# Performance work log

Hardware: AMD Instinct MI355X
Metric: run time of the kernel (lower is better)

## Reference

```python
import jax, jax.numpy as jnp
import numpy as np

R, DIL = 3, 2  # radius, dilation for neighbor correlation


def conv2d(x, w, b):
    # standard 3x3 stride-1 SAME conv, NCHW / OIHW
    y = jax.lax.conv_general_dilated(x, w, (1, 1), 'SAME',
                                     dimension_numbers=('NCHW', 'OIHW', 'NCHW'))
    return y + b[None, :, None, None]


def bilinear_gather(x, py, px):
    # x: (n,c,h,w); py/px: (n,K,h,w) float sampling coords; zero outside bounds
    n, c, h, w = x.shape
    y0 = jnp.floor(py); x0 = jnp.floor(px)
    wy = py - y0; wx = px - x0
    xf = x.reshape(n, c, h * w)

    def gather(yi, xi):
        valid = ((yi >= 0) & (yi < h) & (xi >= 0) & (xi < w)).astype(x.dtype)
        yc = jnp.clip(yi, 0, h - 1).astype(jnp.int32)
        xc = jnp.clip(xi, 0, w - 1).astype(jnp.int32)
        idx = (yc * w + xc).reshape(n, -1)  # (n, K*h*w)
        v = jax.vmap(lambda f, i: f[:, i])(xf, idx)  # (n, c, K*h*w)
        return v.reshape(n, c, *yi.shape[1:]) * valid[:, None]

    v00 = gather(y0, x0); v01 = gather(y0, x0 + 1)
    v10 = gather(y0 + 1, x0); v11 = gather(y0 + 1, x0 + 1)
    wy_ = wy[:, None]; wx_ = wx[:, None]
    return (v00 * (1 - wy_) * (1 - wx_) + v01 * (1 - wy_) * wx_
            + v10 * wy_ * (1 - wx_) + v11 * wy_ * wx_)


def dcn(x, w, b, ow, ob):
    # DCNv2-style modulated deformable 3x3 conv, stride 1, pad 1, 1 deformable group.
    # Offset/mask predicted by an internal conv: channels = [dy(9), dx(9), mask(9)].
    n, c, h, w_ = x.shape
    K = 9
    om = conv2d(x, ow, ob)  # (n, 27, h, w)
    dy, dx = om[:, :K], om[:, K:2 * K]
    mask = jax.nn.sigmoid(om[:, 2 * K:])
    ky, kx = jnp.meshgrid(jnp.arange(-1, 2), jnp.arange(-1, 2), indexing='ij')
    ky = ky.reshape(K).astype(x.dtype); kx = kx.reshape(K).astype(x.dtype)
    yy = jnp.arange(h, dtype=x.dtype)[None, None, :, None]
    xx = jnp.arange(w_, dtype=x.dtype)[None, None, None, :]
    py = yy + ky[None, :, None, None] + dy  # (n,K,h,w)
    px = xx + kx[None, :, None, None] + dx
    samp = bilinear_gather(x, py, px) * mask[:, None]  # (n,c,K,h,w)
    return jnp.einsum('nckhw,ock->nohw', samp, w.reshape(w.shape[0], c, K)) + b[None, :, None, None]


def ncf(f1, f2, radius, dilation):
    # neighbor_correlation_filter: unfold-based sliding-window dot-product attention
    n, c, h, w = f2.shape
    k = 2 * radius + 1
    pad = (k - 1) * dilation // 2
    f2p = jnp.pad(f2, ((0, 0), (0, 0), (pad, pad), (pad, pad)))
    # (n,c,K,h,w), tap order (ky outer, kx inner) matching F.unfold row-major layout
    patches = jnp.stack([f2p[:, :, i * dilation:i * dilation + h, j * dilation:j * dilation + w]
                         for i in range(k) for j in range(k)], axis=2)
    corr = jnp.einsum('nchw,nckhw->nkhw', f1, patches) / jnp.sqrt(jnp.asarray(c, f1.dtype))
    attn = jax.nn.softmax(corr, axis=1)
    sample = jnp.einsum('nkhw,nckhw->nchw', attn, patches)
    return sample, corr


def stargru(x, t, zw, zb, zow, zob, hw, hb, how, hob):
    tx = jnp.concatenate([x, t], axis=1)
    z = jax.nn.sigmoid(dcn(tx, zw, zb, zow, zob))
    r, _ = ncf(t, x, R, DIL)
    xt = jnp.tanh(dcn(jnp.concatenate([r, t], axis=1), hw, hb, how, hob))
    return (1.0 - z) * t + z * xt


def setup_inputs():
    key = jax.random.key(0)
    N, CIN, CH, H, W = 2, 256, 64, 96, 96
    ks = iter(jax.random.split(key, 32))

    def rn(shape, s=0.05):
        return jax.random.normal(next(ks), shape, jnp.float32) * s

    inp = {
        'x': jax.random.normal(next(ks), (N, CIN, H, W), jnp.float32),
        'template': jax.random.normal(next(ks), (N, CH, H, W), jnp.float32),
        'w_in': rn((CH, CIN, 3, 3)), 'b_in': jnp.zeros((CH,), jnp.float32),
        'w_out': rn((CIN, CH, 3, 3)), 'b_out': jnp.zeros((CIN,), jnp.float32),
    }
    for pre in ('enh_z', 'enh_h', 'upd_z', 'upd_h'):
        inp[pre + '_w'] = rn((CH, 2 * CH, 3, 3))
        inp[pre + '_b'] = jnp.zeros((CH,), jnp.float32)
        inp[pre + '_ow'] = rn((27, 2 * CH, 3, 3), 0.01)  # offset/mask conv (small init)
        inp[pre + '_ob'] = jnp.zeros((27,), jnp.float32)
    return inp


def reference(x, template, w_in, b_in, w_out, b_out,
              enh_z_w, enh_z_b, enh_z_ow, enh_z_ob,
              enh_h_w, enh_h_b, enh_h_ow, enh_h_ob,
              upd_z_w, upd_z_b, upd_z_ow, upd_z_ob,
              upd_h_w, upd_h_b, upd_h_ow, upd_h_ob):
    # CrossUpdate forward, post-first-frame branch (self.template is not None)
    xh = conv2d(x, w_in, b_in)
    x_enh = stargru(template, xh,
                    enh_z_w, enh_z_b, enh_z_ow, enh_z_ob,
                    enh_h_w, enh_h_b, enh_h_ow, enh_h_ob)
    new_template = stargru(xh, template,
                           upd_z_w, upd_z_b, upd_z_ow, upd_z_ob,
                           upd_h_w, upd_h_b, upd_h_ow, upd_h_ob)
    out = conv2d(x_enh, w_out, b_out)
    return (out, new_template)
```

## Files before the change

kernel.cpp:

```cpp
#include <hip/hip_runtime.h>
#include <hip/hip_bf16.h>

typedef __hip_bfloat16 bf16;
typedef unsigned short u16;
typedef unsigned int u32;
typedef __attribute__((ext_vector_type(8))) short short8;
typedef __attribute__((ext_vector_type(4))) short bh4;
typedef __attribute__((ext_vector_type(4))) float floatx4;

constexpr int N_ = 2, H_ = 96, W_ = 96, HW_ = H_ * W_;
constexpr int CIN_ = 256, CH_ = 64, C2_ = 128;

__device__ __forceinline__ float sigm(float v) { return 1.0f / (1.0f + __expf(-v)); }
__device__ __forceinline__ short f2b(float v) { bf16 h = __float2bfloat16(v); return *reinterpret_cast<short*>(&h); }
__device__ __forceinline__ float b2f(short s) {
    union { u32 i; float f; } v; v.i = ((u32)(u16)s) << 16; return v.f;
}

constexpr int A_IN_OFF = 0,                         A_IN_SZ  = 64 * 2304;
constexpr int A_OUT_OFF = A_IN_OFF + A_IN_SZ,       A_OUT_SZ = 256 * 576;
constexpr int A_OFF_OFF = A_OUT_OFF + A_OUT_SZ,     A_OFF_SZ = 64 * 1152;
constexpr int A_DCN_OFF = A_OFF_OFF + 4 * A_OFF_SZ, A_DCN_SZ = 64 * 1152;
constexpr int A_TOT = A_DCN_OFF + 4 * A_DCN_SZ;

__global__ __launch_bounds__(256) void cvt_weights(
        const float* __restrict__ w_in, const float* __restrict__ w_out,
        const float* __restrict__ ow0, const float* __restrict__ ow1,
        const float* __restrict__ ow2, const float* __restrict__ ow3,
        const float* __restrict__ w0, const float* __restrict__ w1,
        const float* __restrict__ w2, const float* __restrict__ w3,
        u16* __restrict__ dst) {
    int id = blockIdx.x * 256 + threadIdx.x;
    if (id >= A_TOT) return;
    float v;
    if (id < A_OUT_OFF) {
        int l = id; int m = l / 2304, k = l % 2304; int tap = k >> 8, ic = k & 255;
        v = w_in[m * 2304 + ic * 9 + tap];
    } else if (id < A_OFF_OFF) {
        int l = id - A_OUT_OFF; int m = l / 576, k = l % 576; int tap = k / 64, ic = k & 63;
        v = w_out[m * 576 + ic * 9 + tap];
    } else if (id < A_DCN_OFF) {
        int l = id - A_OFF_OFF; int i = l / A_OFF_SZ, l2 = l % A_OFF_SZ;
        int m = l2 / 1152, k = l2 % 1152; int tap = k >> 7, ic = k & 127;
        const float* s = (i == 0) ? ow0 : (i == 1) ? ow1 : (i == 2) ? ow2 : ow3;
        v = (m < 27) ? s[m * 1152 + ic * 9 + tap] : 0.f;
    } else {
        int l = id - A_DCN_OFF; int i = l / A_DCN_SZ, l2 = l % A_DCN_SZ;
        int m = l2 / 1152, k = l2 % 1152; int tap = k >> 7, c = k & 127;
        const float* s = (i == 0) ? w0 : (i == 1) ? w1 : (i == 2) ? w2 : w3;
        v = s[m * 1152 + c * 9 + tap];
    }
    short sb = f2b(v);
    dst[id] = *reinterpret_cast<u16*>(&sb);
}

__global__ __launch_bounds__(256) void prep(const float* __restrict__ x, const float* __restrict__ tpl,
                                            u16* __restrict__ xT, u16* __restrict__ ta, u16* __restrict__ tb) {
    int id = blockIdx.x * 256 + threadIdx.x;
    constexpr int XIDS = N_ * HW_ * 32;
    if (id < XIDS) {
        int c8 = id & 31;
        int pix = id >> 5;
        int n = pix / HW_, p = pix % HW_;
        const float* s = x + ((size_t)n * 256 + c8 * 8) * HW_ + p;
        short8 vv;
#pragma unroll
        for (int j = 0; j < 8; ++j) vv[j] = f2b(s[(size_t)j * HW_]);
        *reinterpret_cast<short8*>(xT + (size_t)pix * 256 + c8 * 8) = vv;
    } else {
        int id2 = id - XIDS;
        int c8 = id2 & 7;
        int pix = id2 >> 3;
        int n = pix / HW_, p = pix % HW_;
        const float* s = tpl + ((size_t)n * 64 + c8 * 8) * HW_ + p;
        short8 vv;
#pragma unroll
        for (int j = 0; j < 8; ++j) vv[j] = f2b(s[(size_t)j * HW_]);
        *reinterpret_cast<short8*>(ta + (size_t)pix * 128 + c8 * 8) = vv;
        *reinterpret_cast<short8*>(tb + (size_t)pix * 128 + 64 + c8 * 8) = vv;
    }
}

template <int IC, int OCST, int CC>
__device__ __forceinline__ void conv_core(const u16* __restrict__ X,
                                          const u16* __restrict__ A,
                                          const float* __restrict__ bias,
                                          float* __restrict__ out,
                                          u16* __restrict__ ta, u16* __restrict__ tb,
                                          int r, int mt, int t) {
    constexpr int K = IC * 9;
    constexpr int ICC = IC / 64;
    __shared__ __align__(16) u16 Xl[3][50][72];
    int n = r / 192;
    int rr = r % 192;
    int y = rr >> 1, px0 = (rr & 1) * 48;
    int w = t >> 6, lane = t & 63, lm = lane & 15, q = lane >> 4;
    const u16* Arow = A + (size_t)(mt * 64 + w * 16 + lm) * K + q * 8;
    floatx4 acc[3];
#pragma unroll
    for (int a = 0; a < 3; ++a) acc[a] = {0.f, 0.f, 0.f, 0.f};
    const short8 zz = {0, 0, 0, 0, 0, 0, 0, 0};

    for (int icc = 0; icc < ICC; ++icc) {
        short8 af[9][2];
#pragma unroll
        for (int tap = 0; tap < 9; ++tap)
#pragma unroll
            for (int ks = 0; ks < 2; ++ks)
                af[tap][ks] = *reinterpret_cast<const short8*>(Arow + tap * IC + icc * 64 + ks * 32);
        __syncthreads();
#pragma unroll
        for (int it = 0; it < 5; ++it) {
            int id = it * 256 + t;
            if (id < 1200) {
                int ch8 = id & 7;
                int tmp = id >> 3;
                int pxl = tmp % 50, row = tmp / 50;
                int xg = px0 - 1 + pxl;
                int yg = y - 1 + row;
                bool vld = (yg >= 0) && (yg < 96) && (xg >= 0) && (xg < 96);
                short8 vv = zz;
                if (vld)
                    vv = *reinterpret_cast<const short8*>(
                        X + ((size_t)(n * HW_ + yg * 96 + xg)) * IC + icc * 64 + ch8 * 8);
                *reinterpret_cast<short8*>(&Xl[row][pxl][ch8 * 8]) = vv;
            }
        }
        __syncthreads();
#pragma unroll
        for (int tap = 0; tap < 9; ++tap) {
            int ky = tap / 3, kx = tap % 3;
#pragma unroll
            for (int ks = 0; ks < 2; ++ks) {
#pragma unroll
                for (int nf = 0; nf < 3; ++nf) {
                    short8 bv = *reinterpret_cast<const short8*>(&Xl[ky][nf * 16 + lm + kx][ks * 32 + q * 8]);
                    acc[nf] = __builtin_amdgcn_mfma_f32_16x16x32_bf16(af[tap][ks], bv, acc[nf], 0, 0, 0);
                }
            }
        }
    }
    int ocb = mt * 64 + w * 16 + q * 4;
#pragma unroll
    for (int nf = 0; nf < 3; ++nf) {
        int px = px0 + nf * 16 + lm;
        if constexpr (CC) {
            int pix = n * HW_ + y * 96 + px;
            bh4 bo;
#pragma unroll
            for (int rr2 = 0; rr2 < 4; ++rr2) {
                int oc = ocb + rr2;
                float v = acc[nf][rr2] + bias[oc];
                out[((size_t)(n * OCST + oc)) * HW_ + y * 96 + px] = v;
                bo[rr2] = f2b(v);
            }
            *reinterpret_cast<bh4*>(ta + (size_t)pix * 128 + 64 + ocb) = bo;
            *reinterpret_cast<bh4*>(tb + (size_t)pix * 128 + ocb) = bo;
        } else {
#pragma unroll
            for (int rr2 = 0; rr2 < 4; ++rr2) {
                int oc = ocb + rr2;
                if (oc < OCST)
                    out[((size_t)(n * OCST + oc)) * HW_ + y * 96 + px] = acc[nf][rr2] + bias[oc];
            }
        }
    }
}

template <int IC, int OCST, int CC>
__global__ __launch_bounds__(256) void conv_gemm(const u16* __restrict__ X,
                                                 const u16* __restrict__ A,
                                                 const float* __restrict__ bias,
                                                 float* __restrict__ out,
                                                 u16* __restrict__ ta, u16* __restrict__ tb) {
    conv_core<IC, OCST, CC>(X, A, bias, out, ta, tb, blockIdx.x % 384, blockIdx.x / 384, threadIdx.x);
}

template <int GATE>
__global__ __launch_bounds__(256) void od_fused(
        const u16* __restrict__ X0, const u16* __restrict__ X1,
        const u16* __restrict__ Ao0, const u16* __restrict__ Ao1,
        const float* __restrict__ bo0, const float* __restrict__ bo1,
        const u16* __restrict__ Ad0, const u16* __restrict__ Ad1,
        const float* __restrict__ bd0, const float* __restrict__ bd1,
        float* __restrict__ o0, float* __restrict__ o1,
        const float* __restrict__ g0, const float* __restrict__ g1,
        const float* __restrict__ t0, const float* __restrict__ t1,
        u16* __restrict__ xeh, float* __restrict__ ontpl) {
    __shared__ __align__(16) u16 Xl[3][50][72];
    __shared__ float om_l[27][48];
    __shared__ __align__(16) u16 Bl[48][72];
    __shared__ float s_wy[432], s_wx[432], s_m[432];
    __shared__ int s_y0[432], s_x0[432];
    int inst = blockIdx.x / 384, r = blockIdx.x % 384, t = threadIdx.x;
    const u16* X = inst ? X1 : X0;
    const u16* Ao = inst ? Ao1 : Ao0;
    const float* bo = inst ? bo1 : bo0;
    const u16* Ad = inst ? Ad1 : Ad0;
    const float* bd = inst ? bd1 : bd0;
    int n = r / 192, rr = r % 192;
    int y = rr >> 1, px0 = (rr & 1) * 48;
    int w = t >> 6, lane = t & 63, lm = lane & 15, q = lane >> 4;
    const short8 zz = {0, 0, 0, 0, 0, 0, 0, 0};

    {
        const u16* Arow = Ao + (size_t)(w * 16 + lm) * 1152 + q * 8;
        floatx4 acc[3];
#pragma unroll
        for (int a = 0; a < 3; ++a) acc[a] = {0.f, 0.f, 0.f, 0.f};
        for (int icc = 0; icc < 2; ++icc) {
            short8 af[9][2];
#pragma unroll
            for (int tap = 0; tap < 9; ++tap)
#pragma unroll
                for (int ks = 0; ks < 2; ++ks)
                    af[tap][ks] = *reinterpret_cast<const short8*>(Arow + tap * 128 + icc * 64 + ks * 32);
            __syncthreads();
#pragma unroll
            for (int it = 0; it < 5; ++it) {
                int id = it * 256 + t;
                if (id < 1200) {
                    int ch8 = id & 7;
                    int tmp = id >> 3;
                    int pxl = tmp % 50, row = tmp / 50;
                    int xg = px0 - 1 + pxl;
                    int yg = y - 1 + row;
                    bool vld = (yg >= 0) && (yg < 96) && (xg >= 0) && (xg < 96);
                    short8 vv = zz;
                    if (vld)
                        vv = *reinterpret_cast<const short8*>(
                            X + ((size_t)(n * HW_ + yg * 96 + xg)) * 128 + icc * 64 + ch8 * 8);
                    *reinterpret_cast<short8*>(&Xl[row][pxl][ch8 * 8]) = vv;
                }
            }
            __syncthreads();
#pragma unroll
            for (int tap = 0; tap < 9; ++tap) {
                int ky = tap / 3, kx = tap % 3;
#pragma unroll
                for (int ks = 0; ks < 2; ++ks) {
#pragma unroll
                    for (int nf = 0; nf < 3; ++nf) {
                        short8 bv = *reinterpret_cast<const short8*>(&Xl[ky][nf * 16 + lm + kx][ks * 32 + q * 8]);
                        acc[nf] = __builtin_amdgcn_mfma_f32_16x16x32_bf16(af[tap][ks], bv, acc[nf], 0, 0, 0);
                    }
                }
            }
        }
        int ocb = w * 16 + q * 4;
#pragma unroll
        for (int nf = 0; nf < 3; ++nf) {
            int xl = nf * 16 + lm;
#pragma unroll
            for (int rr2 = 0; rr2 < 4; ++rr2) {
                int oc = ocb + rr2;
                if (oc < 27) om_l[oc][xl] = acc[nf][rr2] + bo[oc];
            }
        }
    }
    __syncthreads();

    for (int e = t; e < 432; e += 256) {
        int k9 = e / 48, xl = e % 48;
        int x = px0 + xl;
        float dy = om_l[k9][xl];
        float dx = om_l[9 + k9][xl];
        float ml = om_l[18 + k9][xl];
        float py = (float)y + (float)(k9 / 3 - 1) + dy;
        float px = (float)x + (float)(k9 % 3 - 1) + dx;
        float fy = floorf(py), fx = floorf(px);
        s_y0[e] = (int)fy; s_x0[e] = (int)fx;
        s_wy[e] = py - fy; s_wx[e] = px - fx; s_m[e] = sigm(ml);
    }
    const u16* Arow = Ad + (size_t)(w * 16 + lm) * 1152 + q * 8;
    floatx4 acc[3];
#pragma unroll
    for (int a = 0; a < 3; ++a) acc[a] = {0.f, 0.f, 0.f, 0.f};
    const u16* txn = X + (size_t)n * HW_ * 128;

    for (int kc = 0; kc < 18; ++kc) {
        int tap = kc >> 1, c0 = (kc & 1) * 64;
        short8 af[2];
#pragma unroll
        for (int ks = 0; ks < 2; ++ks)
            af[ks] = *reinterpret_cast<const short8*>(Arow + kc * 64 + ks * 32);
        __syncthreads();
#pragma unroll
        for (int i = 0; i < 2; ++i) {
            int id = i * 256 + t;
            if (id < 384) {
                int px = id >> 3, ch8 = id & 7;
                int ce = tap * 48 + px;
                int y0 = s_y0[ce], x0 = s_x0[ce];
                float wy = s_wy[ce], wx = s_wx[ce], m = s_m[ce];
                float w00 = (1.f - wy) * (1.f - wx) * m;
                float w01 = (1.f - wy) * wx * m;
                float w10 = wy * (1.f - wx) * m;
                float w11 = wy * wx * m;
                bool yv0 = (y0 >= 0) & (y0 < 96), yv1 = (y0 >= -1) & (y0 < 95);
                bool xv0 = (x0 >= 0) & (x0 < 96), xv1 = (x0 >= -1) & (x0 < 95);
                const u16* base = txn + (long)(y0 * 96 + x0) * 128 + c0 + ch8 * 8;
                short8 v00 = (yv0 && xv0) ? *reinterpret_cast<const short8*>(base) : zz;
                short8 v01 = (yv0 && xv1) ? *reinterpret_cast<const short8*>(base + 128) : zz;
                short8 v10 = (yv1 && xv0) ? *reinterpret_cast<const short8*>(base + 96 * 128) : zz;
                short8 v11 = (yv1 && xv1) ? *reinterpret_cast<const short8*>(base + 96 * 128 + 128) : zz;
                short8 vv;
#pragma unroll
                for (int j = 0; j < 8; ++j) {
                    float f = b2f(v00[j]) * w00 + b2f(v01[j]) * w01 +
                              b2f(v10[j]) * w10 + b2f(v11[j]) * w11;
                    vv[j] = f2b(f);
                }
                *reinterpret_cast<short8*>(&Bl[px][ch8 * 8]) = vv;
            }
        }
        __syncthreads();
#pragma unroll
        for (int ks = 0; ks < 2; ++ks)
#pragma unroll
            for (int nf = 0; nf < 3; ++nf) {
                short8 bv = *reinterpret_cast<const short8*>(&Bl[nf * 16 + lm][ks * 32 + q * 8]);
                acc[nf] = __builtin_amdgcn_mfma_f32_16x16x32_bf16(af[ks], bv, acc[nf], 0, 0, 0);
            }
    }
    int ocb = w * 16 + q * 4;
    if constexpr (GATE == 0) {
        float* out = inst ? o1 : o0;
#pragma unroll
        for (int nf = 0; nf < 3; ++nf) {
            int px = px0 + nf * 16 + lm;
#pragma unroll
            for (int rr2 = 0; rr2 < 4; ++rr2) {
                int oc = ocb + rr2;
                out[((size_t)(n * CH_ + oc)) * HW_ + y * 96 + px] = acc[nf][rr2] + bd[oc];
            }
        }
    } else {
        const float* gz = inst ? g1 : g0;
        const float* tt = inst ? t1 : t0;
#pragma unroll
        for (int nf = 0; nf < 3; ++nf) {
            int px = px0 + nf * 16 + lm;
            if (!inst) {
                bh4 bo4;
#pragma unroll
                for (int rr2 = 0; rr2 < 4; ++rr2) {
                    int oc = ocb + rr2;
                    size_t idx = ((size_t)(n * CH_ + oc)) * HW_ + y * 96 + px;
                    float z = sigm(gz[idx]);
                    float xt = tanhf(acc[nf][rr2] + bd[oc]);
                    bo4[rr2] = f2b((1.f - z) * tt[idx] + z * xt);
                }
                *reinterpret_cast<bh4*>(xeh + ((size_t)(n * HW_ + y * 96 + px)) * 64 + ocb) = bo4;
            } else {
#pragma unroll
                for (int rr2 = 0; rr2 < 4; ++rr2) {
                    int oc = ocb + rr2;
                    size_t idx = ((size_t)(n * CH_ + oc)) * HW_ + y * 96 + px;
                    float z = sigm(gz[idx]);
                    float xt = tanhf(acc[nf][rr2] + bd[oc]);
                    ontpl[idx] = (1.f - z) * tt[idx] + z * xt;
                }
            }
        }
    }
}

__global__ __launch_bounds__(256, 4) void ncf2(const u16* __restrict__ in0, const u16* __restrict__ in1,
                                               u16* __restrict__ out0, u16* __restrict__ out1) {
    __shared__ __align__(16) u16 sF2[7][28][72];
    __shared__ __align__(16) u16 sF1[16][72];
    __shared__ float sc[16][52];
    int t = threadIdx.x;
    int inst = blockIdx.x / 1152, bb = blockIdx.x % 1152;
    const u16* txh = inst ? in1 : in0;
    u16* txh2 = inst ? out1 : out0;
    int n = bb / 576, rem = bb % 576;
    int y = rem / 6, x0 = (rem % 6) * 16;
    const u16* base = txh + (size_t)n * HW_ * 128;
    const short8 zz = {0, 0, 0, 0, 0, 0, 0, 0};

    for (int id = t; id < 1568; id += 256) {
        int ch8 = id & 7;
        int tmp = id >> 3;
        int px = tmp % 28, row = tmp / 28;
        int yy = y + row * 2 - 6;
        int xg = x0 - 6 + px;
        short8 vv = zz;
        if (yy >= 0 && yy < 96 && xg >= 0 && xg < 96)
            vv = *reinterpret_cast<const short8*>(base + (size_t)(yy * 96 + xg) * 128 + ch8 * 8);
        *reinterpret_cast<short8*>(&sF2[row][px][ch8 * 8]) = vv;
    }
    if (t < 128) {
        int ch8 = t & 7, lp0 = t >> 3;
        short8 vv = *reinterpret_cast<const short8*>(base + (size_t)(y * 96 + x0 + lp0) * 128 + 64 + ch8 * 8);
        *reinterpret_cast<short8*>(&sF1[lp0][ch8 * 8]) = vv;
    }
    __syncthreads();

    int lp = t >> 4, j = t & 15;
    for (int k = j; k < 49; k += 16) {
        int ky = k / 7, kx = k % 7;
        const u16* f2p = &sF2[ky][lp + 2 * kx][0];
        const u16* f1p = &sF1[lp][0];
        float s = 0.f;
#pragma unroll
        for (int c8 = 0; c8 < 8; ++c8) {
            short8 a = *reinterpret_cast<const short8*>(f1p + c8 * 8);
            short8 b = *reinterpret_cast<const short8*>(f2p + c8 * 8);
#pragma unroll
            for (int u = 0; u < 8; ++u) s += b2f(a[u]) * b2f(b[u]);
        }
        sc[lp][k] = s * 0.125f;
    }
    float mx = -1e30f;
    for (int k = j; k < 49; k += 16) mx = fmaxf(mx, sc[lp][k]);
#pragma unroll
    for (int m = 1; m <= 8; m <<= 1) mx = fmaxf(mx, __shfl_xor(mx, m, 64));
    float e[4];
    float sum = 0.f;
    int cnt = 0;
    for (int k = j; k < 49; k += 16) { e[cnt] = __expf(sc[lp][k] - mx); sum += e[cnt]; ++cnt; }
#pragma unroll
    for (int m = 1; m <= 8; m <<= 1) sum += __shfl_xor(sum, m, 64);
    float inv = 1.f / sum;
    cnt = 0;
    for (int k = j; k < 49; k += 16) sc[lp][k] = e[cnt++] * inv;
    __syncthreads();
    int ch0 = j * 4;
    float acc[4];
#pragma unroll
    for (int u = 0; u < 4; ++u) acc[u] = 0.f;
#pragma unroll
    for (int k = 0; k < 49; ++k) {
        int ky = k / 7, kx = k % 7;
        float a = sc[lp][k];
        bh4 f2 = *reinterpret_cast<const bh4*>(&sF2[ky][lp + 2 * kx][ch0]);
#pragma unroll
        for (int u = 0; u < 4; ++u) acc[u] += a * b2f(f2[u]);
    }
    int p = y * 96 + x0 + lp;
    u16* obase = txh2 + (size_t)n * HW_ * 128 + (size_t)p * 128;
    bh4 ro;
#pragma unroll
    for (int u = 0; u < 4; ++u) ro[u] = f2b(acc[u]);
    *reinterpret_cast<bh4*>(obase + ch0) = ro;
    *reinterpret_cast<bh4*>(obase + 64 + ch0) =
        *reinterpret_cast<const bh4*>(&sF1[lp][ch0]);
}

extern "C" void kernel_launch(void* const* d_in, const int* in_sizes, int n_in,
                              void* d_out, int out_size, void* d_ws, size_t ws_size,
                              hipStream_t stream) {
    const float* x     = (const float*)d_in[0];
    const float* tpl   = (const float*)d_in[1];
    const float* w_in  = (const float*)d_in[2];
    const float* b_in  = (const float*)d_in[3];
    const float* w_out = (const float*)d_in[4];
    const float* b_out = (const float*)d_in[5];
    const float *pw[4], *pb[4], *pow_[4], *pob[4];
    for (int i = 0; i < 4; ++i) {
        pw[i]   = (const float*)d_in[6 + 4 * i];
        pb[i]   = (const float*)d_in[7 + 4 * i];
        pow_[i] = (const float*)d_in[8 + 4 * i];
        pob[i]  = (const float*)d_in[9 + 4 * i];
    }
    float* out_main = (float*)d_out;
    float* out_ntpl = out_main + (size_t)N_ * CIN_ * HW_;

    u16* Aws = (u16*)d_ws;
    u16* xT     = Aws + A_TOT;
    u16* txh_a  = xT + (size_t)N_ * HW_ * CIN_;
    u16* txh_b  = txh_a + (size_t)N_ * HW_ * C2_;
    u16* txh2_a = txh_b + (size_t)N_ * HW_ * C2_;
    u16* txh2_b = txh2_a + (size_t)N_ * HW_ * C2_;
    u16* xeh    = txh2_b + (size_t)N_ * HW_ * C2_;
    float* fws = (float*)(xeh + (size_t)N_ * HW_ * CH_);
    size_t off = 0;
    float* xh   = fws + off; off += (size_t)N_ * CH_ * HW_;
    float* dz_a = fws + off; off += (size_t)N_ * CH_ * HW_;
    float* dz_b = fws + off; off += (size_t)N_ * CH_ * HW_;

    cvt_weights<<<(A_TOT + 255) / 256, 256, 0, stream>>>(
        w_in, w_out, pow_[0], pow_[1], pow_[2], pow_[3], pw[0], pw[1], pw[2], pw[3], Aws);
    prep<<<2880, 256, 0, stream>>>(x, tpl, xT, txh_a, txh_b);
    conv_gemm<CIN_, 64, 1><<<384, 256, 0, stream>>>(xT, Aws + A_IN_OFF, b_in, xh, txh_a, txh_b);

    od_fused<0><<<768, 256, 0, stream>>>(txh_a, txh_b,
        Aws + A_OFF_OFF + 0 * A_OFF_SZ, Aws + A_OFF_OFF + 2 * A_OFF_SZ, pob[0], pob[2],
        Aws + A_DCN_OFF + 0 * A_DCN_SZ, Aws + A_DCN_OFF + 2 * A_DCN_SZ, pb[0], pb[2],
        dz_a, dz_b, nullptr, nullptr, nullptr, nullptr, nullptr, nullptr);

    ncf2<<<2304, 256, 0, stream>>>(txh_a, txh_b, txh2_a, txh2_b);

    od_fused<1><<<768, 256, 0, stream>>>(txh2_a, txh2_b,
        Aws + A_OFF_OFF + 1 * A_OFF_SZ, Aws + A_OFF_OFF + 3 * A_OFF_SZ, pob[1], pob[3],
        Aws + A_DCN_OFF + 1 * A_DCN_SZ, Aws + A_DCN_OFF + 3 * A_DCN_SZ, pb[1], pb[3],
        nullptr, nullptr, dz_a, dz_b, xh, tpl, xeh, out_ntpl);

    conv_gemm<CH_, 256, 0><<<1536, 256, 0, stream>>>(xeh, Aws + A_OUT_OFF, b_out, out_main, nullptr, nullptr);
}
```

Measured before the change: 322.4 us.

## Stage 7x54 input window in LDS for deformable bilinear gathers

The deformable conv now loads a 7-row by 54-column halo window of the input for each 64-channel half into shared memory. Bilinear taps whose offsets fall inside the window read from LDS, and out-of-window samples fall back to global loads. The B tile is double-buffered so only one barrier is needed per tap, and shared memory is manually aliased to fit. This cuts repeated global gather traffic, but it raises LDS use (about 77KB), which can lower occupancy, and it adds the cost of loading the window.

Result: slower. 371.6 us (+15.3%).

```diff
diff --git a/kernel.cpp b/kernel.cpp
--- a/kernel.cpp
+++ b/kernel.cpp
@@ -176,6 +176,9 @@
     conv_core<IC, OCST, CC>(X, A, bias, out, ta, tb, blockIdx.x % 384, blockIdx.x / 384, threadIdx.x);
 }
 
+constexpr int WIN_R = 7, WIN_C = 54, WIN_P = 72;
+constexpr int SM_OM = 21600, SM_S = 54432, SM_BL = 63072, SM_SZ = 76896;
+
 template <int GATE>
 __global__ __launch_bounds__(256) void od_fused(
         const u16* __restrict__ X0, const u16* __restrict__ X1,
@@ -187,11 +190,17 @@
         const float* __restrict__ g0, const float* __restrict__ g1,
         const float* __restrict__ t0, const float* __restrict__ t1,
         u16* __restrict__ xeh, float* __restrict__ ontpl) {
-    __shared__ __align__(16) u16 Xl[3][50][72];
-    __shared__ float om_l[27][48];
-    __shared__ __align__(16) u16 Bl[48][72];
-    __shared__ float s_wy[432], s_wx[432], s_m[432];
-    __shared__ int s_y0[432], s_x0[432];
+    __shared__ __align__(16) char smem[SM_SZ];
+    u16 (*Xl)[50][72] = reinterpret_cast<u16(*)[50][72]>(smem);
+    float (*om_l)[48] = reinterpret_cast<float(*)[48]>(smem + SM_OM);
+    u16 (*sWin)[WIN_C][WIN_P] = reinterpret_cast<u16(*)[WIN_C][WIN_P]>(smem);
+    int* s_y0 = reinterpret_cast<int*>(smem + SM_S);
+    int* s_x0 = s_y0 + 432;
+    float* s_wy = reinterpret_cast<float*>(s_x0 + 432);
+    float* s_wx = s_wy + 432;
+    float* s_m  = s_wx + 432;
+    u16 (*Bl)[48][72] = reinterpret_cast<u16(*)[48][72]>(smem + SM_BL);
+
     int inst = blockIdx.x / 384, r = blockIdx.x % 384, t = threadIdx.x;
     const u16* X = inst ? X1 : X0;
     const u16* Ao = inst ? Ao1 : Ao0;
@@ -272,57 +281,86 @@
         s_y0[e] = (int)fy; s_x0[e] = (int)fx;
         s_wy[e] = py - fy; s_wx[e] = px - fx; s_m[e] = sigm(ml);
     }
+    __syncthreads();
+
     const u16* Arow = Ad + (size_t)(w * 16 + lm) * 1152 + q * 8;
     floatx4 acc[3];
 #pragma unroll
     for (int a = 0; a < 3; ++a) acc[a] = {0.f, 0.f, 0.f, 0.f};
     const u16* txn = X + (size_t)n * HW_ * 128;
-
-    for (int kc = 0; kc < 18; ++kc) {
-        int tap = kc >> 1, c0 = (kc & 1) * 64;
-        short8 af[2];
-#pragma unroll
-        for (int ks = 0; ks < 2; ++ks)
-            af[ks] = *reinterpret_cast<const short8*>(Arow + kc * 64 + ks * 32);
+    int p = 0;
+
+    for (int half = 0; half < 2; ++half) {
+        int c0 = half * 64;
+        for (int id = t; id < WIN_R * WIN_C * 8; id += 256) {
+            int ch8 = id & 7;
+            int tmp = id >> 3;
+            int col = tmp % WIN_C, row = tmp / WIN_C;
+            int gy = y - 3 + row, gx = px0 - 3 + col;
+            short8 vv = zz;
+            if (gy >= 0 && gy < 96 && gx >= 0 && gx < 96)
+                vv = *reinterpret_cast<const short8*>(txn + (size_t)(gy * 96 + gx) * 128 + c0 + ch8 * 8);
+            *reinterpret_cast<short8*>(&sWin[row][col][ch8 * 8]) = vv;
+        }
         __syncthreads();
-#pragma unroll
-        for (int i = 0; i < 2; ++i) {
-            int id = i * 256 + t;
-            if (id < 384) {
-                int px = id >> 3, ch8 = id & 7;
-                int ce = tap * 48 + px;
-                int y0 = s_y0[ce], x0 = s_x0[ce];
-                float wy = s_wy[ce], wx = s_wx[ce], m = s_m[ce];
-                float w00 = (1.f - wy) * (1.f - wx) * m;
-                float w01 = (1.f - wy) * wx * m;
-                float w10 = wy * (1.f - wx) * m;
-                float w11 = wy * wx * m;
-                bool yv0 = (y0 >= 0) & (y0 < 96), yv1 = (y0 >= -1) & (y0 < 95);
-                bool xv0 = (x0 >= 0) & (x0 < 96), xv1 = (x0 >= -1) & (x0 < 95);
-                const u16* base = txn + (long)(y0 * 96 + x0) * 128 + c0 + ch8 * 8;
-                short8 v00 = (yv0 && xv0) ? *reinterpret_cast<const short8*>(base) : zz;
-                short8 v01 = (yv0 && xv1) ? *reinterpret_cast<const short8*>(base + 128) : zz;
-                short8 v10 = (yv1 && xv0) ? *reinterpret_cast<const short8*>(base + 96 * 128) : zz;
-                short8 v11 = (yv1 && xv1) ? *reinterpret_cast<const short8*>(base + 96 * 128 + 128) : zz;
-                short8 vv;
-#pragma unroll
-                for (int j = 0; j < 8; ++j) {
-                    float f = b2f(v00[j]) * w00 + b2f(v01[j]) * w01 +
-                              b2f(v10[j]) * w10 + b2f(v11[j]) * w11;
-                    vv[j] = f2b(f);
-                }
-                *reinterpret_cast<short8*>(&Bl[px][ch8 * 8]) = vv;
-            }
-        }
-        __syncthreads();
-#pragma unroll
-        for (int ks = 0; ks < 2; ++ks)
-#pragma unroll
-            for (int nf = 0; nf < 3; ++nf) {
-                short8 bv = *reinterpret_cast<const short8*>(&Bl[nf * 16 + lm][ks * 32 + q * 8]);
-                acc[nf] = __builtin_amdgcn_mfma_f32_16x16x32_bf16(af[ks], bv, acc[nf], 0, 0, 0);
-            }
-    }
+        for (int tap = 0; tap < 9; ++tap) {
+            short8 af[2];
+#pragma unroll
+            for (int ks = 0; ks < 2; ++ks)
+                af[ks] = *reinterpret_cast<const short8*>(Arow + tap * 128 + c0 + ks * 32);
+#pragma unroll
+            for (int i = 0; i < 2; ++i) {
+                int id = i * 256 + t;
+                if (id < 384) {
+                    int px = id >> 3, ch8 = id & 7;
+                    int ce = tap * 48 + px;
+                    int y0 = s_y0[ce], x0c = s_x0[ce];
+                    float wy = s_wy[ce], wx = s_wx[ce], m = s_m[ce];
+                    float w00 = (1.f - wy) * (1.f - wx) * m;
+                    float w01 = (1.f - wy) * wx * m;
+                    float w10 = wy * (1.f - wx) * m;
+                    float w11 = wy * wx * m;
+                    int rl = y0 - y + 3;
+                    int cl = x0c - px0 + 3;
+                    short8 v00, v01, v10, v11;
+                    if ((u32)rl < 6u && (u32)cl < 53u) {
+                        const u16* wp = &sWin[rl][cl][ch8 * 8];
+                        v00 = *reinterpret_cast<const short8*>(wp);
+                        v01 = *reinterpret_cast<const short8*>(wp + WIN_P);
+                        v10 = *reinterpret_cast<const short8*>(wp + WIN_C * WIN_P);
+                        v11 = *reinterpret_cast<const short8*>(wp + WIN_C * WIN_P + WIN_P);
+                    } else {
+                        bool yv0 = (y0 >= 0) & (y0 < 96), yv1 = (y0 >= -1) & (y0 < 95);
+                        bool xv0 = (x0c >= 0) & (x0c < 96), xv1 = (x0c >= -1) & (x0c < 95);
+                        const u16* gb = txn + (long)(y0 * 96 + x0c) * 128 + c0 + ch8 * 8;
+                        v00 = (yv0 && xv0) ? *reinterpret_cast<const short8*>(gb) : zz;
+                        v01 = (yv0 && xv1) ? *reinterpret_cast<const short8*>(gb + 128) : zz;
+                        v10 = (yv1 && xv0) ? *reinterpret_cast<const short8*>(gb + 96 * 128) : zz;
+                        v11 = (yv1 && xv1) ? *reinterpret_cast<const short8*>(gb + 96 * 128 + 128) : zz;
+                    }
+                    short8 vv;
+#pragma unroll
+                    for (int j = 0; j < 8; ++j) {
+                        float f = b2f(v00[j]) * w00 + b2f(v01[j]) * w01 +
+                                  b2f(v10[j]) * w10 + b2f(v11[j]) * w11;
+                        vv[j] = f2b(f);
+                    }
+                    *reinterpret_cast<short8*>(&Bl[p][px][ch8 * 8]) = vv;
+                }
+            }
+            __syncthreads();
+#pragma unroll
+            for (int ks = 0; ks < 2; ++ks)
+#pragma unroll
+                for (int nf = 0; nf < 3; ++nf) {
+                    short8 bv = *reinterpret_cast<const short8*>(&Bl[p][nf * 16 + lm][ks * 32 + q * 8]);
+                    acc[nf] = __builtin_amdgcn_mfma_f32_16x16x32_bf16(af[ks], bv, acc[nf], 0, 0, 0);
+                }
+            p ^= 1;
+        }
+        if (half == 0) __syncthreads();
+    }
+
     int ocb = w * 16 + q * 4;
     if constexpr (GATE == 0) {
         float* out = inst ? o1 : o0;
```

## Double-buffer deformable gather with register prefetch and remap blocks for XCD locality

Applied to the files above, without the earlier changes.

The DCN main loop in od_fused is software-pipelined. Bilinear corner loads for the next chunk are issued into registers while the current chunk is blended into one of two LDS buffers and the previous buffer feeds the MFMAs, leaving one barrier per iteration instead of two. Separately, block indices in conv_gemm, od_fused and ncf2 are permuted with an 8-way interleave so that neighbouring tiles land on the same XCD and share L2. The pipelining adds register pressure (eight short8 prefetch registers per thread) and doubles the Bl LDS buffer, which could lower occupancy.

New measurement: 310.6 us. 1.04x faster.

```diff
diff --git a/kernel.cpp b/kernel.cpp
--- a/kernel.cpp
+++ b/kernel.cpp
@@ -173,7 +173,9 @@
                                                  const float* __restrict__ bias,
                                                  float* __restrict__ out,
                                                  u16* __restrict__ ta, u16* __restrict__ tb) {
-    conv_core<IC, OCST, CC>(X, A, bias, out, ta, tb, blockIdx.x % 384, blockIdx.x / 384, threadIdx.x);
+    int cpx = gridDim.x >> 3;
+    int b = (blockIdx.x & 7) * cpx + (blockIdx.x >> 3);
+    conv_core<IC, OCST, CC>(X, A, bias, out, ta, tb, b % 384, b / 384, threadIdx.x);
 }
 
 template <int GATE>
@@ -189,10 +191,13 @@
         u16* __restrict__ xeh, float* __restrict__ ontpl) {
     __shared__ __align__(16) u16 Xl[3][50][72];
     __shared__ float om_l[27][48];
-    __shared__ __align__(16) u16 Bl[48][72];
+    __shared__ __align__(16) u16 Bl[2][48][72];
     __shared__ float s_wy[432], s_wx[432], s_m[432];
     __shared__ int s_y0[432], s_x0[432];
-    int inst = blockIdx.x / 384, r = blockIdx.x % 384, t = threadIdx.x;
+
+    int bid = blockIdx.x;
+    int b = (bid & 7) * 96 + (bid >> 3);
+    int inst = b / 384, r = b % 384, t = threadIdx.x;
     const u16* X = inst ? X1 : X0;
     const u16* Ao = inst ? Ao1 : Ao0;
     const float* bo = inst ? bo1 : bo0;
@@ -272,57 +277,80 @@
         s_y0[e] = (int)fy; s_x0[e] = (int)fx;
         s_wy[e] = py - fy; s_wx[e] = px - fx; s_m[e] = sigm(ml);
     }
+    __syncthreads();
+
     const u16* Arow = Ad + (size_t)(w * 16 + lm) * 1152 + q * 8;
     floatx4 acc[3];
 #pragma unroll
     for (int a = 0; a < 3; ++a) acc[a] = {0.f, 0.f, 0.f, 0.f};
     const u16* txn = X + (size_t)n * HW_ * 128;
-
+    int p = 0;
+    bool active = (t < 192);
+    short8 cA[4], cB[4];
+    short8 afP[2];
+
+    auto issueI = [&](int kc_, int id, short8* cr) {
+        int tap = kc_ >> 1, c0 = (kc_ & 1) * 64;
+        int px = id >> 3, ch8 = id & 7;
+        int ce = tap * 48 + px;
+        int y0 = s_y0[ce], x0c = s_x0[ce];
+        bool yv0 = (y0 >= 0) & (y0 < 96), yv1 = (y0 >= -1) & (y0 < 95);
+        bool xv0 = (x0c >= 0) & (x0c < 96), xv1 = (x0c >= -1) & (x0c < 95);
+        const u16* gb = txn + (long)(y0 * 96 + x0c) * 128 + c0 + ch8 * 8;
+        cr[0] = (yv0 && xv0) ? *reinterpret_cast<const short8*>(gb) : zz;
+        cr[1] = (yv0 && xv1) ? *reinterpret_cast<const short8*>(gb + 128) : zz;
+        cr[2] = (yv1 && xv0) ? *reinterpret_cast<const short8*>(gb + 96 * 128) : zz;
+        cr[3] = (yv1 && xv1) ? *reinterpret_cast<const short8*>(gb + 96 * 128 + 128) : zz;
+    };
+    auto computeI = [&](int kc_, int id, const short8* cr) {
+        int tap = kc_ >> 1;
+        int px = id >> 3, ch8 = id & 7;
+        int ce = tap * 48 + px;
+        float wy = s_wy[ce], wx = s_wx[ce], m = s_m[ce];
+        float w00 = (1.f - wy) * (1.f - wx) * m;
+        float w01 = (1.f - wy) * wx * m;
+        float w10 = wy * (1.f - wx) * m;
+        float w11 = wy * wx * m;
+        short8 vv;
+#pragma unroll
+        for (int j = 0; j < 8; ++j) {
+            float f = b2f(cr[0][j]) * w00 + b2f(cr[1][j]) * w01 +
+                      b2f(cr[2][j]) * w10 + b2f(cr[3][j]) * w11;
+            vv[j] = f2b(f);
+        }
+        *reinterpret_cast<short8*>(&Bl[p][px][ch8 * 8]) = vv;
+    };
+
+    if (active) { issueI(0, t, cA); issueI(0, t + 192, cB); }
     for (int kc = 0; kc < 18; ++kc) {
-        int tap = kc >> 1, c0 = (kc & 1) * 64;
-        short8 af[2];
+        if (kc > 0) {
+#pragma unroll
+            for (int ks = 0; ks < 2; ++ks)
+#pragma unroll
+                for (int nf = 0; nf < 3; ++nf) {
+                    short8 bv = *reinterpret_cast<const short8*>(&Bl[p ^ 1][nf * 16 + lm][ks * 32 + q * 8]);
+                    acc[nf] = __builtin_amdgcn_mfma_f32_16x16x32_bf16(afP[ks], bv, acc[nf], 0, 0, 0);
+                }
+        }
+        if (active) {
+            computeI(kc, t, cA);
+            computeI(kc, t + 192, cB);
+            if (kc < 17) { issueI(kc + 1, t, cA); issueI(kc + 1, t + 192, cB); }
+        }
 #pragma unroll
         for (int ks = 0; ks < 2; ++ks)
-            af[ks] = *reinterpret_cast<const short8*>(Arow + kc * 64 + ks * 32);
+            afP[ks] = *reinterpret_cast<const short8*>(Arow + kc * 64 + ks * 32);
         __syncthreads();
-#pragma unroll
-        for (int i = 0; i < 2; ++i) {
-            int id = i * 256 + t;
-            if (id < 384) {
-                int px = id >> 3, ch8 = id & 7;
-                int ce = tap * 48 + px;
-                int y0 = s_y0[ce], x0 = s_x0[ce];
-                float wy = s_wy[ce], wx = s_wx[ce], m = s_m[ce];
-                float w00 = (1.f - wy) * (1.f - wx) * m;
-                float w01 = (1.f - wy) * wx * m;
-                float w10 = wy * (1.f - wx) * m;
-                float w11 = wy * wx * m;
-                bool yv0 = (y0 >= 0) & (y0 < 96), yv1 = (y0 >= -1) & (y0 < 95);
-                bool xv0 = (x0 >= 0) & (x0 < 96), xv1 = (x0 >= -1) & (x0 < 95);
-                const u16* base = txn + (long)(y0 * 96 + x0) * 128 + c0 + ch8 * 8;
-                short8 v00 = (yv0 && xv0) ? *reinterpret_cast<const short8*>(base) : zz;
-                short8 v01 = (yv0 && xv1) ? *reinterpret_cast<const short8*>(base + 128) : zz;
-                short8 v10 = (yv1 && xv0) ? *reinterpret_cast<const short8*>(base + 96 * 128) : zz;
-                short8 v11 = (yv1 && xv1) ? *reinterpret_cast<const short8*>(base + 96 * 128 + 128) : zz;
-                short8 vv;
-#pragma unroll
-                for (int j = 0; j < 8; ++j) {
-                    float f = b2f(v00[j]) * w00 + b2f(v01[j]) * w01 +
-                              b2f(v10[j]) * w10 + b2f(v11[j]) * w11;
-                    vv[j] = f2b(f);
-                }
-                *reinterpret_cast<short8*>(&Bl[px][ch8 * 8]) = vv;
-            }
-        }
-        __syncthreads();
-#pragma unroll
-        for (int ks = 0; ks < 2; ++ks)
-#pragma unroll
-            for (int nf = 0; nf < 3; ++nf) {
-                short8 bv = *reinterpret_cast<const short8*>(&Bl[nf * 16 + lm][ks * 32 + q * 8]);
-                acc[nf] = __builtin_amdgcn_mfma_f32_16x16x32_bf16(af[ks], bv, acc[nf], 0, 0, 0);
-            }
-    }
+        p ^= 1;
+    }
+#pragma unroll
+    for (int ks = 0; ks < 2; ++ks)
+#pragma unroll
+        for (int nf = 0; nf < 3; ++nf) {
+            short8 bv = *reinterpret_cast<const short8*>(&Bl[p ^ 1][nf * 16 + lm][ks * 32 + q * 8]);
+            acc[nf] = __builtin_amdgcn_mfma_f32_16x16x32_bf16(afP[ks], bv, acc[nf], 0, 0, 0);
+        }
+
     int ocb = w * 16 + q * 4;
     if constexpr (GATE == 0) {
         float* out = inst ? o1 : o0;
@@ -372,7 +400,9 @@
     __shared__ __align__(16) u16 sF1[16][72];
     __shared__ float sc[16][52];
     int t = threadIdx.x;
-    int inst = blockIdx.x / 1152, bb = blockIdx.x % 1152;
+    int bid = blockIdx.x;
+    int b = (bid & 7) * 288 + (bid >> 3);
+    int inst = b / 1152, bb = b % 1152;
     const u16* txh = inst ? in1 : in0;
     u16* txh2 = inst ? out1 : out0;
     int n = bb / 576, rem = bb % 576;
@@ -407,9 +437,9 @@
 #pragma unroll
         for (int c8 = 0; c8 < 8; ++c8) {
             short8 a = *reinterpret_cast<const short8*>(f1p + c8 * 8);
-            short8 b = *reinterpret_cast<const short8*>(f2p + c8 * 8);
-#pragma unroll
-            for (int u = 0; u < 8; ++u) s += b2f(a[u]) * b2f(b[u]);
+            short8 b2 = *reinterpret_cast<const short8*>(f2p + c8 * 8);
+#pragma unroll
+            for (int u = 0; u < 8; ++u) s += b2f(a[u]) * b2f(b2[u]);
         }
         sc[lp][k] = s * 0.125f;
     }
```
